# Performance work log

Measured on AMD Instinct MI355X. Metric: run time of the kernel, lower is better.

Reference implementation:

```python
import jax, jax.numpy as jnp
import numpy as np

CHEB_K = 3
ORDER = 2


def setup_inputs() -> dict:
    key = jax.random.key(0)
    ks = jax.random.split(key, 7)
    B, C, N, T = 16, 64, 2048, 12
    E, O = 10, 64
    x = jax.random.normal(ks[0], (B, C, N, T), jnp.float32)
    node_embeddings = jax.random.normal(ks[1], (N, E), jnp.float32)
    # nonnegative row-normalized adjacency for the diffusion branch
    a = jax.random.uniform(ks[2], (1, N, N), jnp.float32)
    support = a / jnp.sum(a, axis=-1, keepdims=True)
    weights_pool = 0.05 * jax.random.normal(ks[3], (E, CHEB_K, C, O), jnp.float32)
    bias_pool = 0.05 * jax.random.normal(ks[4], (E, O), jnp.float32)
    mlp_w = 0.05 * jax.random.normal(ks[5], ((ORDER * 1 + 1) * C, O), jnp.float32)
    mlp_b = 0.05 * jax.random.normal(ks[6], (O,), jnp.float32)
    return {
        "x": x,
        "node_embeddings": node_embeddings,
        "support": support,
        "weights_pool": weights_pool,
        "bias_pool": bias_pool,
        "mlp_w": mlp_w,
        "mlp_b": mlp_b,
    }


def reference(x, node_embeddings, support, weights_pool, bias_pool, mlp_w, mlp_b):
    # ---- adaptive Chebyshev branch ----
    N = node_embeddings.shape[0]
    A = jax.nn.softmax(jax.nn.relu(node_embeddings @ node_embeddings.T), axis=1)  # [N,N]
    supports = [jnp.eye(N, dtype=A.dtype), A]
    for _ in range(2, CHEB_K):
        supports.append(2.0 * (A @ supports[-1]) - supports[-2])
    S = jnp.stack(supports, axis=0)                         # [K,N,N]
    weights = jnp.einsum('nd,dkio->nkio', node_embeddings, weights_pool)  # [N,K,C,O]
    bias = node_embeddings @ bias_pool                      # [N,O]
    # x: [B,C,N,T]; diffuse then contract per-node weights
    x_g = jnp.einsum('knm,bimw->bwnki', S, x)               # [B,T,N,K,C]
    x_av = jnp.einsum('bwnki,nkio->bwno', x_g, weights) + bias  # [B,T,N,O]
    x_av = x_av.transpose(0, 3, 2, 1)                       # [B,O,N,T]

    # ---- diffusion conv branch ----
    out = [x]
    for si in range(support.shape[0]):
        a = support[si]                                     # [N,N]
        x1 = jnp.einsum('bcvl,vw->bcwl', x, a)
        out.append(x1)
        for _ in range(2, ORDER + 1):
            x1 = jnp.einsum('bcvl,vw->bcwl', x1, a)
            out.append(x1)
    xg = jnp.concatenate(out, axis=1)                       # [B,(order*S+1)*C,N,T]
    # 1x1 Conv2d == channel matmul; dropout is identity in eval mode
    x_gcn = jnp.einsum('bcnw,co->bonw', xg, mlp_w) + mlp_b[None, :, None, None]
    return x_av, x_gcn
```

## Files before the change

kernel.cpp:

```cpp
#include <hip/hip_runtime.h>
#include <stdint.h>

#define NN    2048
#define BB    16
#define CC    64
#define TT    12
#define OO    64
#define ED    10
#define JJ    12288
#define NJ    25165824
#define KC    192
#define NTK   32

typedef __attribute__((ext_vector_type(8))) short short8;
typedef __attribute__((ext_vector_type(4))) float f32x4;

__device__ __forceinline__ unsigned short f2bf(float x) {
    union { float f; unsigned int u; } v; v.f = x;
    unsigned int r = (v.u + 0x7FFFu + ((v.u >> 16) & 1u)) >> 16;
    return (unsigned short)r;
}
__device__ __forceinline__ float bf2f(unsigned short h) {
    union { unsigned int u; float f; } v; v.u = ((unsigned int)h) << 16;
    return v.f;
}
__device__ __forceinline__ void async_cp16(const void* g, void* l) {
    __builtin_amdgcn_global_load_lds(
        (const __attribute__((address_space(1))) void*)(uintptr_t)g,
        (__attribute__((address_space(3))) void*)(uintptr_t)l, 16, 0, 0);
}

__global__ __launch_bounds__(256) void k_softmax_A(const float* __restrict__ E,
                                                   unsigned short* __restrict__ Abf) {
    int n = blockIdx.x, tid = threadIdx.x;
    __shared__ float row[NN];
    __shared__ float red[256];
    float en[ED];
#pragma unroll
    for (int d = 0; d < ED; ++d) en[d] = E[n * ED + d];
    float mx = 0.0f;
    for (int m = tid; m < NN; m += 256) {
        float s = 0.f;
#pragma unroll
        for (int d = 0; d < ED; ++d) s += en[d] * E[m * ED + d];
        s = fmaxf(s, 0.0f);
        row[m] = s;
        mx = fmaxf(mx, s);
    }
    red[tid] = mx; __syncthreads();
    for (int s = 128; s; s >>= 1) { if (tid < s) red[tid] = fmaxf(red[tid], red[tid + s]); __syncthreads(); }
    mx = red[0]; __syncthreads();
    float sum = 0.f;
    for (int m = tid; m < NN; m += 256) { float e = __expf(row[m] - mx); row[m] = e; sum += e; }
    red[tid] = sum; __syncthreads();
    for (int s = 128; s; s >>= 1) { if (tid < s) red[tid] += red[tid + s]; __syncthreads(); }
    float inv = 1.0f / red[0];
    for (int m = tid; m < NN; m += 256) Abf[(size_t)n * NN + m] = f2bf(row[m] * inv);
}

__global__ void k_trans_bf(const float* __restrict__ src, unsigned short* __restrict__ dst) {
    __shared__ float t[32][33];
    int tx = threadIdx.x, ty = threadIdx.y;
    int x0 = blockIdx.x * 32, y0 = blockIdx.y * 32;
#pragma unroll
    for (int i = 0; i < 4; ++i)
        t[ty + i * 8][tx] = src[(size_t)(y0 + ty + i * 8) * NN + x0 + tx];
    __syncthreads();
#pragma unroll
    for (int i = 0; i < 4; ++i)
        dst[(size_t)(x0 + ty + i * 8) * NN + y0 + tx] = f2bf(t[tx][ty + i * 8]);
}

__global__ __launch_bounds__(256) void k_make_X2(const float* __restrict__ x,
                                                 unsigned short* __restrict__ X2) {
    int idx = blockIdx.x * 256 + threadIdx.x;
    int n = idx / JJ;
    int r = idx - n * JJ;
    int bt = r >> 6;
    int c = r & 63;
    int b = bt / TT;
    int t = bt - b * TT;
    X2[idx] = f2bf(x[(((size_t)b * CC + c) * NN + n) * TT + t]);
}

__global__ __launch_bounds__(256) void k_trans16(const unsigned short* __restrict__ src,
                                                 unsigned short* __restrict__ dst) {
    __shared__ unsigned short t[64][72];
    int tid = threadIdx.x;
    int j0 = blockIdx.x * 64, n0 = blockIdx.y * 64;
    int r = tid >> 3, c8 = (tid & 7) * 8;
#pragma unroll
    for (int it = 0; it < 2; ++it) {
        int rr = r + it * 32;
        *(short8*)&t[rr][c8] = *(const short8*)&src[(size_t)(n0 + rr) * JJ + j0 + c8];
    }
    __syncthreads();
#pragma unroll
    for (int it = 0; it < 2; ++it) {
        int rr = r + it * 32;
        unsigned short v[8];
#pragma unroll
        for (int u = 0; u < 8; ++u) v[u] = t[c8 + u][rr];
        *(short8*)&dst[(size_t)(j0 + rr) * NN + n0 + c8] = *(short8*)v;
    }
}

template <int AOFF, int BOFF>
__device__ __forceinline__ void mfma_quad(f32x4 (&acc)[8][4],
                                          const short8 (&A)[4][2],
                                          const short8 (&B)[2][2]) {
    __builtin_amdgcn_s_setprio(1);
#pragma unroll
    for (int h = 0; h < 2; ++h)
#pragma unroll
        for (int tm = 0; tm < 4; ++tm)
#pragma unroll
            for (int tn = 0; tn < 2; ++tn)
                acc[AOFF + tm][BOFF + tn] = __builtin_amdgcn_mfma_f32_16x16x32_bf16(
                    A[tm][h], B[tn][h], acc[AOFF + tm][BOFF + tn], 0, 0, 0);
    __builtin_amdgcn_s_setprio(0);
}

__global__ __launch_bounds__(512, 2) void k_gemm8(const unsigned short* __restrict__ AmA,
                                                  const unsigned short* __restrict__ AmB,
                                                  const unsigned short* __restrict__ Bt,
                                                  unsigned short* __restrict__ OutA,
                                                  unsigned short* __restrict__ OutB,
                                                  const unsigned short* __restrict__ Csub,
                                                  float alpha) {
    extern __shared__ char ldsc[];
    int tid = threadIdx.x, lane = tid & 63, wv = tid >> 6;
    int q = lane >> 4, l15 = lane & 15;

    const unsigned short* Am = blockIdx.z ? AmB : AmA;
    unsigned short* Out      = blockIdx.z ? OutB : OutA;

    int j0g = blockIdx.x * 256, m0g = blockIdx.y * 256;

    int wmw = (wv >> 2) * 128;
    int wnw = (wv & 3) * 64;

    int srow = tid >> 3;
    int scol = ((tid & 7) * 16) ^ ((srow & 7) << 4);
    const char* srcA0 = (const char*)Am + (size_t)(m0g + srow) * 4096 + scol;
    const char* srcB0 = (const char*)Bt + (size_t)(j0g + srow) * 4096 + scol;
    char* dstA0 = ldsc + tid * 16;
    char* dstB0 = ldsc + 32768 + tid * 16;

#define STAGE_A(nb, kt, h)                                                                  \
    do {                                                                                    \
        async_cp16(srcA0 + (size_t)(kt) * 128 + (h) * 524288,                               \
                   dstA0 + (nb) * 65536 + (h) * 16384);                                     \
        async_cp16(srcA0 + (size_t)(kt) * 128 + (h) * 524288 + 262144,                      \
                   dstA0 + (nb) * 65536 + (h) * 16384 + 8192);                              \
    } while (0)
#define STAGE_B(nb, kt, h)                                                                  \
    do {                                                                                    \
        async_cp16(srcB0 + (size_t)(kt) * 128 + (h) * 524288,                               \
                   dstB0 + (nb) * 65536 + (h) * 16384);                                     \
        async_cp16(srcB0 + (size_t)(kt) * 128 + (h) * 524288 + 262144,                      \
                   dstB0 + (nb) * 65536 + (h) * 16384 + 8192);                              \
    } while (0)

    int rsw = (l15 & 7) << 4;
    int colh0 = (q * 16) ^ rsw;
    int colh1 = colh0 ^ 64;
    int arA = (wmw + l15) * 128;
    int arB = (wnw + l15) * 128;

    f32x4 acc[8][4];
#pragma unroll
    for (int a = 0; a < 8; ++a)
#pragma unroll
        for (int b = 0; b < 4; ++b) acc[a][b] = (f32x4){0.f, 0.f, 0.f, 0.f};

    STAGE_A(0, 0, 0);
    STAGE_A(0, 0, 1);
    STAGE_B(0, 0, 0);
    STAGE_B(0, 0, 1);
    STAGE_B(1, 1, 0);
    STAGE_B(1, 1, 1);
    asm volatile("s_waitcnt vmcnt(4)" ::: "memory");
    __builtin_amdgcn_s_barrier();
    asm volatile("" ::: "memory");

    int cur = 0;
    for (int t = 0; t < NTK; ++t, cur ^= 1) {
        const int nb = cur ^ 1;
        const char* pa = ldsc + (cur << 16);
        const char* pA0 = pa + arA;
        const char* pB0 = pa + 32768 + arB;

        if (t + 1 < NTK) {
            STAGE_A(nb, t + 1, 0);
            STAGE_A(nb, t + 1, 1);
        }

        short8 af[4][2], bf0[2][2], bf1[2][2];

#pragma unroll
        for (int tm = 0; tm < 4; ++tm) {
            af[tm][0] = *(const short8*)(pA0 + tm * 2048 + colh0);
            af[tm][1] = *(const short8*)(pA0 + tm * 2048 + colh1);
        }
#pragma unroll
        for (int tn = 0; tn < 2; ++tn) {
            bf0[tn][0] = *(const short8*)(pB0 + tn * 2048 + colh0);
            bf0[tn][1] = *(const short8*)(pB0 + tn * 2048 + colh1);
            bf1[tn][0] = *(const short8*)(pB0 + 4096 + tn * 2048 + colh0);
            bf1[tn][1] = *(const short8*)(pB0 + 4096 + tn * 2048 + colh1);
        }
        mfma_quad<0, 0>(acc, af, bf0);
        mfma_quad<0, 2>(acc, af, bf1);

        if (t + 2 < NTK) {
            asm volatile("s_waitcnt lgkmcnt(0)" ::: "memory");
            __builtin_amdgcn_s_barrier();
            asm volatile("" ::: "memory");
            STAGE_B(cur, t + 2, 0);
            STAGE_B(cur, t + 2, 1);
        }

#pragma unroll
        for (int tm = 0; tm < 4; ++tm) {
            af[tm][0] = *(const short8*)(pA0 + 8192 + tm * 2048 + colh0);
            af[tm][1] = *(const short8*)(pA0 + 8192 + tm * 2048 + colh1);
        }
        mfma_quad<4, 2>(acc, af, bf1);
        mfma_quad<4, 0>(acc, af, bf0);

        if (t + 2 < NTK) {
            asm volatile("s_waitcnt vmcnt(4) lgkmcnt(0)" ::: "memory");
            __builtin_amdgcn_s_barrier();
            asm volatile("" ::: "memory");
        } else if (t + 1 < NTK) {
            asm volatile("s_waitcnt vmcnt(0) lgkmcnt(0)" ::: "memory");
            __builtin_amdgcn_s_barrier();
            asm volatile("" ::: "memory");
        }
    }
#undef STAGE_A
#undef STAGE_B

#pragma unroll
    for (int a = 0; a < 8; ++a) {
        int mbase = m0g + wmw + (a >> 2) * 64 + (a & 3) * 16 + q * 4;
#pragma unroll
        for (int b = 0; b < 4; ++b) {
            int jj = j0g + wnw + (b >> 1) * 32 + (b & 1) * 16 + l15;
#pragma unroll
            for (int r = 0; r < 4; ++r) {
                size_t oidx = (size_t)(mbase + r) * JJ + jj;
                float v = alpha * acc[a][b][r];
                if (Csub) v -= bf2f(Csub[oidx]);
                Out[oidx] = f2bf(v);
            }
        }
    }
}

__global__ __launch_bounds__(256) void k_node(const unsigned short* __restrict__ S0,
                                              const unsigned short* __restrict__ S1,
                                              const unsigned short* __restrict__ S2,
                                              const float* __restrict__ E,
                                              const float* __restrict__ Wp,
                                              const float* __restrict__ bias_pool,
                                              const float* __restrict__ mlp_w,
                                              const float* __restrict__ mlp_b,
                                              float* __restrict__ out,
                                              int branch) {
    int n = blockIdx.x, tid = threadIdx.x, lane = tid & 63, wv = tid >> 6;
    __shared__ __align__(16) unsigned short lW[64 * 200];
    __shared__ __align__(16) unsigned short lS[192 * 72];
    __shared__ float lBias[64];
    int q = lane >> 4, l15 = lane & 15;

    if (branch == 0) {
        float en[ED];
#pragma unroll
        for (int d = 0; d < ED; ++d) en[d] = E[n * ED + d];
        for (int idx = tid; idx < KC * OO; idx += 256) {
            int o = idx & 63, kap = idx >> 6;
            float s = 0.f;
#pragma unroll
            for (int d = 0; d < ED; ++d) s += en[d] * Wp[((size_t)d * KC + kap) * OO + o];
            lW[o * 200 + kap] = f2bf(s);
        }
        if (tid < 64) {
            float s = 0.f;
#pragma unroll
            for (int d = 0; d < ED; ++d) s += en[d] * bias_pool[d * OO + tid];
            lBias[tid] = s;
        }
    } else {
        for (int idx = tid; idx < KC * OO; idx += 256) {
            int o = idx & 63, kap = idx >> 6;
            lW[o * 200 + kap] = f2bf(mlp_w[kap * OO + o]);
        }
        if (tid < 64) lBias[tid] = mlp_b[tid];
    }

    f32x4 zero = {0.f, 0.f, 0.f, 0.f};
    f32x4 acc[3][4];
#pragma unroll
    for (int a = 0; a < 3; ++a)
#pragma unroll
        for (int b = 0; b < 4; ++b) acc[a][b] = zero;

    const unsigned short* Ss[3] = { S0 + (size_t)n * JJ, S1 + (size_t)n * JJ, S2 + (size_t)n * JJ };

    for (int s = 0; s < 3; ++s) {
        __syncthreads();
#pragma unroll
        for (int v = 0; v < 6; ++v) {
            int e8 = (v * 256 + tid) * 8;
            int m = e8 >> 6, i = e8 & 63;
            *(short8*)&lS[m * 72 + i] = *(const short8*)&Ss[s][e8];
        }
        __syncthreads();
#pragma unroll
        for (int h = 0; h < 2; ++h) {
            short8 af[3], bfr[4];
#pragma unroll
            for (int tm = 0; tm < 3; ++tm)
                af[tm] = *(const short8*)&lS[(wv * 48 + tm * 16 + l15) * 72 + h * 32 + q * 8];
#pragma unroll
            for (int tn = 0; tn < 4; ++tn)
                bfr[tn] = *(const short8*)&lW[(tn * 16 + l15) * 200 + s * 64 + h * 32 + q * 8];
#pragma unroll
            for (int tm = 0; tm < 3; ++tm)
#pragma unroll
                for (int tn = 0; tn < 4; ++tn)
                    acc[tm][tn] = __builtin_amdgcn_mfma_f32_16x16x32_bf16(af[tm], bfr[tn], acc[tm][tn], 0, 0, 0);
        }
    }
#pragma unroll
    for (int tm = 0; tm < 3; ++tm) {
#pragma unroll
        for (int tn = 0; tn < 4; ++tn) {
            int o = tn * 16 + l15;
#pragma unroll
            for (int r = 0; r < 4; ++r) {
                int m = wv * 48 + tm * 16 + q * 4 + r;
                int b = m / TT, t = m - b * TT;
                out[(((size_t)b * OO + o) * NN + n) * TT + t] = acc[tm][tn][r] + lBias[o];
            }
        }
    }
}

extern "C" void kernel_launch(void* const* d_in, const int* in_sizes, int n_in,
                              void* d_out, int out_size, void* d_ws, size_t ws_size,
                              hipStream_t stream) {
    const float* x         = (const float*)d_in[0];
    const float* node_emb  = (const float*)d_in[1];
    const float* support   = (const float*)d_in[2];
    const float* wpool     = (const float*)d_in[3];
    const float* bpool     = (const float*)d_in[4];
    const float* mlp_w     = (const float*)d_in[5];
    const float* mlp_b     = (const float*)d_in[6];
    float* out             = (float*)d_out;

    unsigned short* Abf = (unsigned short*)d_ws;
    unsigned short* Atb = Abf + (size_t)NN * NN;
    unsigned short* b1  = Atb + (size_t)NN * NN;
    unsigned short* b2  = b1 + (size_t)NJ;
    unsigned short* b3  = b2 + (size_t)NJ;
    unsigned short* b4  = b3 + (size_t)NJ;
    unsigned short* b5  = b4 + (size_t)NJ;

    static int attr_done = 0;
    if (!attr_done) {
        hipFuncSetAttribute(reinterpret_cast<const void*>(k_gemm8),
                            hipFuncAttributeMaxDynamicSharedMemorySize, 131072);
        attr_done = 1;
    }

    dim3 gg13(48, 8, 2);
    dim3 gg1(48, 8, 1);
    dim3 gt(192, 32);

    k_softmax_A<<<NN, 256, 0, stream>>>(node_emb, Abf);
    k_trans_bf<<<dim3(64, 64), dim3(32, 8), 0, stream>>>(support, Atb);
    k_make_X2<<<NJ / 256, 256, 0, stream>>>(x, b2);
    k_trans16<<<gt, 256, 0, stream>>>(b2, b1);

    k_gemm8<<<gg13, 512, 131072, stream>>>(Abf, Atb, b1, b4, b5, nullptr, 1.0f);

    k_trans16<<<gt, 256, 0, stream>>>(b4, b3);
    k_gemm8<<<gg1, 512, 131072, stream>>>(Abf, Abf, b3, b1, b1, b2, 2.0f);
    k_node<<<NN, 256, 0, stream>>>(b2, b4, b1, node_emb, wpool, bpool, nullptr, nullptr,
                                   out, 0);

    k_trans16<<<gt, 256, 0, stream>>>(b5, b3);
    k_gemm8<<<gg1, 512, 131072, stream>>>(Atb, Atb, b3, b4, b4, nullptr, 1.0f);
    k_node<<<NN, 256, 0, stream>>>(b2, b5, b4, nullptr, nullptr, nullptr, mlp_w, mlp_b,
                                   out + (size_t)NJ, 1);
}
```

Before: 1.080 ms.

## Fold Chebyshev recurrence into node weights and fuse X layout+transpose kernel

The Chebyshev term 2*A*(A x) - x is no longer formed in the GEMM epilogue. The third support is fed as raw A*(A x), and the subtraction and doubling are folded into the per-node weight generation (W0-W2, W1, 2*W2). This removes the Csub read and the scaling from the GEMM epilogue. Separately, a new LDS-staged kernel builds both the bf16 node-major X2 and its transpose in one pass, replacing the element-wise conversion plus a separate transpose kernel. The trade-off is extra global loads during weight generation and a large LDS footprint that limits occupancy of the fused conversion kernel.

```diff
diff --git a/kernel.cpp b/kernel.cpp
--- a/kernel.cpp
+++ b/kernel.cpp
@@ -71,16 +71,46 @@
         dst[(size_t)(x0 + ty + i * 8) * NN + y0 + tx] = f2bf(t[tx][ty + i * 8]);
 }
 
-__global__ __launch_bounds__(256) void k_make_X2(const float* __restrict__ x,
-                                                 unsigned short* __restrict__ X2) {
-    int idx = blockIdx.x * 256 + threadIdx.x;
-    int n = idx / JJ;
-    int r = idx - n * JJ;
-    int bt = r >> 6;
-    int c = r & 63;
-    int b = bt / TT;
-    int t = bt - b * TT;
-    X2[idx] = f2bf(x[(((size_t)b * CC + c) * NN + n) * TT + t]);
+__global__ __launch_bounds__(256) void k_make_X2b(const float* __restrict__ x,
+                                                  unsigned short* __restrict__ X2,
+                                                  unsigned short* __restrict__ X2t) {
+    extern __shared__ float lx[];
+    int b = blockIdx.x, n0 = blockIdx.y * 32, tid = threadIdx.x;
+#pragma unroll
+    for (int v = 0; v < 24; ++v) {
+        int f4 = v * 256 + tid;
+        int c = f4 / 96, r4 = f4 - c * 96;
+        const float4* src = (const float4*)(x + ((size_t)(b * CC + c) * NN + n0) * TT) + r4;
+        float4 val = *src;
+#pragma unroll
+        for (int u = 0; u < 4; ++u) {
+            int idx = r4 * 4 + u;
+            int n = idx / 12, t = idx - n * 12;
+            lx[c * 417 + n * 13 + t] = ((const float*)&val)[u];
+        }
+    }
+    __syncthreads();
+#pragma unroll
+    for (int v = 0; v < 12; ++v) {
+        int flat = v * 256 + tid;
+        int n = flat / 96, u8 = flat - n * 96;
+        int jl = u8 * 8;
+        int t = jl >> 6, c0 = jl & 63;
+        unsigned short w[8];
+#pragma unroll
+        for (int e = 0; e < 8; ++e) w[e] = f2bf(lx[(c0 + e) * 417 + n * 13 + t]);
+        *(short8*)&X2[(size_t)(n0 + n) * JJ + b * 768 + jl] = *(short8*)w;
+    }
+#pragma unroll
+    for (int v = 0; v < 12; ++v) {
+        int flat = v * 256 + tid;
+        int jl = flat >> 2, nq = (flat & 3) * 8;
+        int t = jl >> 6, c = jl & 63;
+        unsigned short w[8];
+#pragma unroll
+        for (int e = 0; e < 8; ++e) w[e] = f2bf(lx[c * 417 + (nq + e) * 13 + t]);
+        *(short8*)&X2t[(size_t)(b * 768 + jl) * NN + n0 + nq] = *(short8*)w;
+    }
 }
 
 __global__ __launch_bounds__(256) void k_trans16(const unsigned short* __restrict__ src,
@@ -125,9 +155,7 @@
                                                   const unsigned short* __restrict__ AmB,
                                                   const unsigned short* __restrict__ Bt,
                                                   unsigned short* __restrict__ OutA,
-                                                  unsigned short* __restrict__ OutB,
-                                                  const unsigned short* __restrict__ Csub,
-                                                  float alpha) {
+                                                  unsigned short* __restrict__ OutB) {
     extern __shared__ char ldsc[];
     int tid = threadIdx.x, lane = tid & 63, wv = tid >> 6;
     int q = lane >> 4, l15 = lane & 15;
@@ -251,9 +279,7 @@
 #pragma unroll
             for (int r = 0; r < 4; ++r) {
                 size_t oidx = (size_t)(mbase + r) * JJ + jj;
-                float v = alpha * acc[a][b][r];
-                if (Csub) v -= bf2f(Csub[oidx]);
-                Out[oidx] = f2bf(v);
+                Out[oidx] = f2bf(acc[a][b][r]);
             }
         }
     }
@@ -281,9 +307,19 @@
         for (int d = 0; d < ED; ++d) en[d] = E[n * ED + d];
         for (int idx = tid; idx < KC * OO; idx += 256) {
             int o = idx & 63, kap = idx >> 6;
+            int k = kap >> 6, i = kap & 63;
             float s = 0.f;
 #pragma unroll
-            for (int d = 0; d < ED; ++d) s += en[d] * Wp[((size_t)d * KC + kap) * OO + o];
+            for (int d = 0; d < ED; ++d) {
+                float w;
+                if (k == 0)
+                    w = Wp[((size_t)d * KC + i) * OO + o] - Wp[((size_t)d * KC + 128 + i) * OO + o];
+                else if (k == 1)
+                    w = Wp[((size_t)d * KC + 64 + i) * OO + o];
+                else
+                    w = 2.0f * Wp[((size_t)d * KC + 128 + i) * OO + o];
+                s += en[d] * w;
+            }
             lW[o * 200 + kap] = f2bf(s);
         }
         if (tid < 64) {
@@ -373,6 +409,8 @@
     if (!attr_done) {
         hipFuncSetAttribute(reinterpret_cast<const void*>(k_gemm8),
                             hipFuncAttributeMaxDynamicSharedMemorySize, 131072);
+        hipFuncSetAttribute(reinterpret_cast<const void*>(k_make_X2b),
+                            hipFuncAttributeMaxDynamicSharedMemorySize, 106752);
         attr_done = 1;
     }
 
@@ -382,18 +420,17 @@
 
     k_softmax_A<<<NN, 256, 0, stream>>>(node_emb, Abf);
     k_trans_bf<<<dim3(64, 64), dim3(32, 8), 0, stream>>>(support, Atb);
-    k_make_X2<<<NJ / 256, 256, 0, stream>>>(x, b2);
-    k_trans16<<<gt, 256, 0, stream>>>(b2, b1);
-
-    k_gemm8<<<gg13, 512, 131072, stream>>>(Abf, Atb, b1, b4, b5, nullptr, 1.0f);
+    k_make_X2b<<<dim3(16, 64), 256, 106752, stream>>>(x, b2, b1);
+
+    k_gemm8<<<gg13, 512, 131072, stream>>>(Abf, Atb, b1, b4, b5);
 
     k_trans16<<<gt, 256, 0, stream>>>(b4, b3);
-    k_gemm8<<<gg1, 512, 131072, stream>>>(Abf, Abf, b3, b1, b1, b2, 2.0f);
+    k_gemm8<<<gg1, 512, 131072, stream>>>(Abf, Abf, b3, b1, b1);
     k_node<<<NN, 256, 0, stream>>>(b2, b4, b1, node_emb, wpool, bpool, nullptr, nullptr,
                                    out, 0);
 
     k_trans16<<<gt, 256, 0, stream>>>(b5, b3);
-    k_gemm8<<<gg1, 512, 131072, stream>>>(Atb, Atb, b3, b4, b4, nullptr, 1.0f);
+    k_gemm8<<<gg1, 512, 131072, stream>>>(Atb, Atb, b3, b4, b4);
     k_node<<<NN, 256, 0, stream>>>(b2, b5, b4, nullptr, nullptr, nullptr, mlp_w, mlp_b,
                                    out + (size_t)NJ, 1);
 }
```

Result: slower. 1.153 ms (+6.8%).
